# Performance work log

Hardware: AMD Instinct MI355X
Metric: run time of the kernel (lower is better)

The kernel has to match this reference:

```python
import jax, jax.numpy as jnp
import numpy as np

B, N, C = 4, 2048, 768
H = 12
D = C // H  # head_dim = 64
SCALE = D ** -0.5


def setup_inputs() -> dict:
    key = jax.random.key(0)
    ks = jax.random.split(key, 9)
    x_q = jax.random.normal(ks[0], (B, N, C), dtype=jnp.float32)
    x_k = jax.random.normal(ks[1], (B, N, C), dtype=jnp.float32)
    x_v = jax.random.normal(ks[2], (B, N, C), dtype=jnp.float32)
    x_u = jax.random.uniform(ks[3], (B, N, C), dtype=jnp.float32)
    s = C ** -0.5
    Wq = jax.random.normal(ks[4], (C, C), dtype=jnp.float32) * s
    Wk = jax.random.normal(ks[5], (C, C), dtype=jnp.float32) * s
    Wv = jax.random.normal(ks[6], (C, C), dtype=jnp.float32) * s
    Wp = jax.random.normal(ks[7], (C, C), dtype=jnp.float32) * s
    bp = jax.random.normal(ks[8], (C,), dtype=jnp.float32) * 0.01
    return {"x_q": x_q, "x_k": x_k, "x_v": x_v, "x_u": x_u,
            "Wq": Wq, "Wk": Wk, "Wv": Wv, "Wp": Wp, "bp": bp}


def reference(x_q, x_k, x_v, x_u, Wq, Wk, Wv, Wp, bp):
    # Linear projections (torch Linear: y = x @ W.T), split into heads [B,H,N,D]
    def to_heads(x, W):
        y = jnp.einsum('bnc,oc->bno', x, W)
        return y.reshape(B, N, H, D).transpose(0, 2, 1, 3)
    q = to_heads(x_q, Wq) * SCALE
    k = to_heads(x_k, Wk)
    v = to_heads(x_v, Wv)
    # Scores [B,H,N,N]
    attn = jnp.einsum('bhqd,bhkd->bhqk', q, k)
    # Uncertainty map: per-query scalar (mean over channels), broadcast over keys & heads
    uc = jnp.mean(x_u, axis=-1)  # [B,N]
    attn = attn * uc[:, None, :, None]
    attn = jax.nn.softmax(attn, axis=-1)
    out = jnp.einsum('bhqk,bhkd->bhqd', attn, v)
    out = out.transpose(0, 2, 1, 3).reshape(B, N, C)
    return jnp.einsum('bnc,oc->bno', out, Wp) + bp
```

## Files before the change

### kernel.cpp

```cpp
#include <hip/hip_runtime.h>
#include <hip/hip_bf16.h>
#include <cstdint>

#define B_ 4
#define N_ 2048
#define C_ 768
#define H_ 12
#define D_ 64
#define QSCALE 0.18033688011112042f

typedef __bf16 bf16x8 __attribute__((ext_vector_type(8)));
typedef float f32x4 __attribute__((ext_vector_type(4)));
typedef float f32x16 __attribute__((ext_vector_type(16)));

__device__ __forceinline__ unsigned f2bs(float x) {
  unsigned u = __builtin_bit_cast(unsigned, x);
  unsigned r = (u + 0x7fffu + ((u >> 16) & 1u)) >> 16;
  return r;
}

__device__ __forceinline__ bf16x8 ldb8(const unsigned short* p) {
  return __builtin_bit_cast(bf16x8, *(const uint4*)p);
}

__device__ __forceinline__ f32x4 mfma16(bf16x8 a, bf16x8 b, f32x4 c) {
  return __builtin_amdgcn_mfma_f32_16x16x32_bf16(a, b, c, 0, 0, 0);
}

__device__ __forceinline__ f32x16 mfma32(bf16x8 a, bf16x8 b, f32x16 c) {
  return __builtin_amdgcn_mfma_f32_32x32x16_bf16(a, b, c, 0, 0, 0);
}

__device__ __forceinline__ void async16(const unsigned short* g, unsigned short* l) {
  __builtin_amdgcn_global_load_lds(
      (const __attribute__((address_space(1))) unsigned int*)g,
      (__attribute__((address_space(3))) unsigned int*)l, 16, 0, 0);
}

__global__ void prep_kernel(
    const float* __restrict__ xq, const float* __restrict__ xk,
    const float* __restrict__ xv, const float* __restrict__ xu,
    const float* __restrict__ Wq, const float* __restrict__ Wk,
    const float* __restrict__ Wv, const float* __restrict__ Wp,
    unsigned short* __restrict__ dxq, unsigned short* __restrict__ dxk,
    unsigned short* __restrict__ dxv,
    unsigned short* __restrict__ dwq, unsigned short* __restrict__ dwk,
    unsigned short* __restrict__ dwv, unsigned short* __restrict__ dwp,
    float* __restrict__ uc) {
  const int id = blockIdx.x;
  if (id < 18432) {
    const float* s = (id < 6144) ? xq : (id < 12288) ? xk : xv;
    unsigned short* d = (id < 6144) ? dxq : (id < 12288) ? dxk : dxv;
    int i = ((id % 6144) * 256 + threadIdx.x) * 4;
    float4 v = *(const float4*)(s + i);
    ushort4 h;
    h.x = (unsigned short)f2bs(v.x); h.y = (unsigned short)f2bs(v.y);
    h.z = (unsigned short)f2bs(v.z); h.w = (unsigned short)f2bs(v.w);
    *(ushort4*)(d + i) = h;
  } else if (id < 20736) {
    int sub = id - 18432;
    int which = sub / 576;
    const float* s = (which == 0) ? Wq : (which == 1) ? Wk : (which == 2) ? Wv : Wp;
    unsigned short* d = (which == 0) ? dwq : (which == 1) ? dwk : (which == 2) ? dwv : dwp;
    int i = ((sub % 576) * 256 + threadIdx.x) * 4;
    float4 v = *(const float4*)(s + i);
    ushort4 h;
    h.x = (unsigned short)f2bs(v.x); h.y = (unsigned short)f2bs(v.y);
    h.z = (unsigned short)f2bs(v.z); h.w = (unsigned short)f2bs(v.w);
    *(ushort4*)(d + i) = h;
  } else {
    int sub = id - 20736;
    int w = threadIdx.x >> 6, lane = threadIdx.x & 63;
    int row = sub * 4 + w;
    const float* p = xu + (size_t)row * C_;
    float s = 0.f;
#pragma unroll
    for (int i = 0; i < 3; ++i) {
      float4 v = *(const float4*)(p + (i * 64 + lane) * 4);
      s += v.x + v.y + v.z + v.w;
    }
#pragma unroll
    for (int off = 1; off < 64; off <<= 1) s += __shfl_xor(s, off);
    if (lane == 0) uc[row] = s * (1.f / 768.f);
  }
}

__device__ __forceinline__ void gemm_mainloop(
    const unsigned short* __restrict__ A, const unsigned short* __restrict__ W,
    int m0, int n0, unsigned short* Al, unsigned short* Bl,
    int tid, int wm, int wn, int quad, int id15, f32x4 (*acc)[4]) {
  const int wb = tid & 192;
  const unsigned short* ap[4];
  const unsigned short* bp[4];
#pragma unroll
  for (int s = 0; s < 4; ++s) {
    int g = s * 256 + tid;
    int row = (g >> 2) & 127;
    int col = ((g >> 9) << 5) | ((g & 3) << 3);
    ap[s] = A + (size_t)(m0 + row) * C_ + col;
    bp[s] = W + (size_t)(n0 + row) * C_ + col;
  }

  for (int kt = 0; kt < C_; kt += 64) {
    __syncthreads();
#pragma unroll
    for (int s = 0; s < 4; ++s) {
      async16(ap[s] + kt, Al + (s * 256 + wb) * 8);
      async16(bp[s] + kt, Bl + (s * 256 + wb) * 8);
    }
    __syncthreads();

#pragma unroll
    for (int kk = 0; kk < 2; ++kk) {
      bf16x8 af[4], bfr[4];
#pragma unroll
      for (int i = 0; i < 4; ++i)
        af[i]  = ldb8(&Al[kk * 4096 + (wm + i * 16 + id15) * 32 + quad * 8]);
#pragma unroll
      for (int j = 0; j < 4; ++j)
        bfr[j] = ldb8(&Bl[kk * 4096 + (wn + j * 16 + id15) * 32 + quad * 8]);
#pragma unroll
      for (int i = 0; i < 4; ++i)
#pragma unroll
        for (int j = 0; j < 4; ++j)
          acc[i][j] = mfma16(af[i], bfr[j], acc[i][j]);
    }
  }
}

#define TSTR 136
__global__ __launch_bounds__(256, 3) void gemm_qkv(
    const unsigned short* __restrict__ xq, const unsigned short* __restrict__ xk,
    const unsigned short* __restrict__ xv,
    const unsigned short* __restrict__ wq, const unsigned short* __restrict__ wk,
    const unsigned short* __restrict__ wv,
    unsigned short* __restrict__ oq, unsigned short* __restrict__ ok,
    unsigned short* __restrict__ ov, const float* __restrict__ uc) {
  __shared__ __align__(16) unsigned short S[128 * TSTR];
  unsigned short* Al = S;
  unsigned short* Bl = S + 8192;
  const int tid = threadIdx.x;
  const int w = tid >> 6, lane = tid & 63, quad = lane >> 4, id15 = lane & 15;
  const int wm = (w >> 1) << 6, wn = (w & 1) << 6;
  const int id = blockIdx.x;
  const int xcd = id & 7, slot = id >> 3;
  const int n0 = (slot % 6) << 7;
  const int gz = xcd * 24 + slot / 6;
  const int z = gz >> 6, m0 = (gz & 63) << 7;

  const unsigned short* A = (z == 0) ? xq : (z == 1) ? xk : xv;
  const unsigned short* W = (z == 0) ? wq : (z == 1) ? wk : wv;

  f32x4 acc[4][4] = {};
  gemm_mainloop(A, W, m0, n0, Al, Bl, tid, wm, wn, quad, id15, acc);

  if (z == 2) {
    __syncthreads();
#pragma unroll
    for (int i = 0; i < 4; ++i)
#pragma unroll
      for (int j = 0; j < 4; ++j) {
        uint2 u;
        u.x = f2bs(acc[i][j][0]) | (f2bs(acc[i][j][1]) << 16);
        u.y = f2bs(acc[i][j][2]) | (f2bs(acc[i][j][3]) << 16);
        *(uint2*)&S[(wn + j * 16 + id15) * TSTR + wm + i * 16 + quad * 4] = u;
      }
    __syncthreads();
    const int b = m0 >> 11, nb = m0 & (N_ - 1);
#pragma unroll
    for (int s = 0; s < 8; ++s) {
      int c = s * 256 + tid;
      int row = c >> 4, o = (c & 15) << 3;
      *(uint4*)(ov + (size_t)(b * C_ + n0 + row) * N_ + nb + o) = *(const uint4*)&S[row * TSTR + o];
    }
    return;
  }

#pragma unroll
  for (int i = 0; i < 4; ++i) {
#pragma unroll
    for (int j = 0; j < 4; ++j) {
#pragma unroll
      for (int r = 0; r < 4; ++r) {
        int gm = m0 + wm + i * 16 + quad * 4 + r;
        int gn = n0 + wn + j * 16 + id15;
        float v = acc[i][j][r];
        if (z == 0) {
          v *= QSCALE * uc[gm];
          oq[(size_t)gm * C_ + gn] = (unsigned short)f2bs(v);
        } else {
          ok[(size_t)gm * C_ + gn] = (unsigned short)f2bs(v);
        }
      }
    }
  }
}

__global__ __launch_bounds__(256, 4) void gemm_out(
    const unsigned short* __restrict__ ao, const unsigned short* __restrict__ wp,
    float* __restrict__ out, const float* __restrict__ bias) {
  __shared__ __align__(16) unsigned short Al[64 * 64];
  __shared__ __align__(16) unsigned short Bl[128 * 64];
  const int tid = threadIdx.x;
  const int w = tid >> 6, lane = tid & 63, quad = lane >> 4, id15 = lane & 15;
  const int wm = (w >> 1) << 5, wn = (w & 1) << 6;
  const int id = blockIdx.x;
  const int xcd = id & 7, slot = id >> 3;
  const int n0 = (slot % 6) << 7;
  const int m0 = (xcd * 16 + slot / 6) << 6;

  const int wb = tid & 192;
  const unsigned short* ap[2];
#pragma unroll
  for (int s = 0; s < 2; ++s) {
    int g = s * 256 + tid;
    int row = (g >> 2) & 63;
    int col = ((g >> 8) << 5) | ((g & 3) << 3);
    ap[s] = ao + (size_t)(m0 + row) * C_ + col;
  }
  const unsigned short* bp[4];
#pragma unroll
  for (int s = 0; s < 4; ++s) {
    int g = s * 256 + tid;
    int row = (g >> 2) & 127;
    int col = ((g >> 9) << 5) | ((g & 3) << 3);
    bp[s] = wp + (size_t)(n0 + row) * C_ + col;
  }

  f32x4 acc[2][4] = {};
  for (int kt = 0; kt < C_; kt += 64) {
    __syncthreads();
#pragma unroll
    for (int s = 0; s < 2; ++s) async16(ap[s] + kt, Al + (s * 256 + wb) * 8);
#pragma unroll
    for (int s = 0; s < 4; ++s) async16(bp[s] + kt, Bl + (s * 256 + wb) * 8);
    __syncthreads();

#pragma unroll
    for (int kk = 0; kk < 2; ++kk) {
      bf16x8 af[2], bfr[4];
#pragma unroll
      for (int i = 0; i < 2; ++i)
        af[i]  = ldb8(&Al[kk * 2048 + (wm + i * 16 + id15) * 32 + quad * 8]);
#pragma unroll
      for (int j = 0; j < 4; ++j)
        bfr[j] = ldb8(&Bl[kk * 4096 + (wn + j * 16 + id15) * 32 + quad * 8]);
#pragma unroll
      for (int i = 0; i < 2; ++i)
#pragma unroll
        for (int j = 0; j < 4; ++j)
          acc[i][j] = mfma16(af[i], bfr[j], acc[i][j]);
    }
  }

#pragma unroll
  for (int i = 0; i < 2; ++i) {
#pragma unroll
    for (int j = 0; j < 4; ++j) {
#pragma unroll
      for (int r = 0; r < 4; ++r) {
        int gm = m0 + wm + i * 16 + quad * 4 + r;
        int gn = n0 + wn + j * 16 + id15;
        out[(size_t)gm * C_ + gn] = acc[i][j][r] + bias[gn];
      }
    }
  }
}

#define KSTR 72
#define VOFF (64 * KSTR)
#define BUFO (2 * 64 * KSTR)
__global__ __launch_bounds__(256, 3) void attn_kernel(
    const unsigned short* __restrict__ Q, const unsigned short* __restrict__ Kk,
    const unsigned short* __restrict__ Vt, unsigned short* __restrict__ O) {
  __shared__ __align__(16) unsigned short KV[2 * 2 * 64 * KSTR];

  const int tid = threadIdx.x;
  const int w = tid >> 6, lane = tid & 63;
  const int i32 = lane & 31, hi = lane >> 5;
  const int id = blockIdx.x;
  const int xcd = id & 7, slot = id >> 3;
  const int bh = xcd * 6 + (slot >> 4);
  const int qt = slot & 15;
  const int b = bh / H_, h = bh % H_;
  const int q0 = qt * 128 + w * 32;

  bf16x8 qf[4];
#pragma unroll
  for (int s = 0; s < 4; ++s)
    qf[s] = ldb8(Q + (size_t)(b * N_ + q0 + i32) * C_ + h * 64 + s * 16 + hi * 8);

  const uint4 onesu = {0x3F803F80u, 0x3F803F80u, 0x3F803F80u, 0x3F803F80u};
  const bf16x8 onesf = __builtin_bit_cast(bf16x8, onesu);

  f32x16 oacc0 = {}, oacc1 = {}, lacc = {};

  const size_t kbase = (size_t)(b * N_) * C_ + h * 64;
  const size_t vbase = (size_t)(b * C_ + h * 64) * N_;
  const int srow0 = tid >> 3, srow1 = 32 + (tid >> 3);
  const int sseg = (tid & 7) << 3;
  const int addrLow = i32 << 2;
  const int addrHigh = addrLow | 128;

  auto compute = [&](const unsigned short* Kc) {
    const unsigned short* Vc = Kc + VOFF;
#pragma unroll
    for (int t = 0; t < 2; ++t) {
      f32x16 s16 = {};
#pragma unroll
      for (int s = 0; s < 4; ++s) {
        bf16x8 kf = ldb8(Kc + (t * 32 + i32) * KSTR + s * 16 + hi * 8);
        s16 = mfma32(kf, qf[s], s16);
      }
      unsigned Dw[8];
#pragma unroll
      for (int j = 0; j < 8; ++j) {
        float e0 = exp2f(s16[2 * j]);
        float e1 = exp2f(s16[2 * j + 1]);
        unsigned d;
        asm("v_cvt_pk_bf16_f32 %0, %1, %2" : "=v"(d) : "v"(e0), "v"(e1));
        Dw[j] = d;
      }
#pragma unroll
      for (int sl = 0; sl < 2; ++sl) {
        const int bb = sl * 4;
        unsigned L2 = (unsigned)__builtin_amdgcn_ds_bpermute(addrLow, (int)Dw[bb + 2]);
        unsigned L3 = (unsigned)__builtin_amdgcn_ds_bpermute(addrLow, (int)Dw[bb + 3]);
        unsigned H0 = (unsigned)__builtin_amdgcn_ds_bpermute(addrHigh, (int)Dw[bb + 0]);
        unsigned H1 = (unsigned)__builtin_amdgcn_ds_bpermute(addrHigh, (int)Dw[bb + 1]);
        uint4 u;
        u.x = hi ? L2 : Dw[bb + 0];
        u.y = hi ? L3 : Dw[bb + 1];
        u.z = hi ? Dw[bb + 2] : H0;
        u.w = hi ? Dw[bb + 3] : H1;
        bf16x8 pf = __builtin_bit_cast(bf16x8, u);
        lacc = mfma32(pf, onesf, lacc);
        bf16x8 v0 = ldb8(Vc + i32 * KSTR + (2 * t + sl) * 16 + hi * 8);
        bf16x8 v1 = ldb8(Vc + (32 + i32) * KSTR + (2 * t + sl) * 16 + hi * 8);
        oacc0 = mfma32(pf, v0, oacc0);
        oacc1 = mfma32(pf, v1, oacc1);
      }
    }
  };

  {
    uint4 a0 = *(const uint4*)(Kk + kbase + (size_t)srow0 * C_ + sseg);
    uint4 a1 = *(const uint4*)(Kk + kbase + (size_t)srow1 * C_ + sseg);
    uint4 c0 = *(const uint4*)(Vt + vbase + (size_t)srow0 * N_ + sseg);
    uint4 c1 = *(const uint4*)(Vt + vbase + (size_t)srow1 * N_ + sseg);
    *(uint4*)&KV[srow0 * KSTR + sseg] = a0;
    *(uint4*)&KV[srow1 * KSTR + sseg] = a1;
    *(uint4*)&KV[VOFF + srow0 * KSTR + sseg] = c0;
    *(uint4*)&KV[VOFF + srow1 * KSTR + sseg] = c1;
  }

  int cur = 0;
  for (int kc = 0; kc < N_ - 64; kc += 64) {
    const int kcn = kc + 64;
    uint4 a0 = *(const uint4*)(Kk + kbase + (size_t)(kcn + srow0) * C_ + sseg);
    uint4 a1 = *(const uint4*)(Kk + kbase + (size_t)(kcn + srow1) * C_ + sseg);
    uint4 c0 = *(const uint4*)(Vt + vbase + (size_t)srow0 * N_ + kcn + sseg);
    uint4 c1 = *(const uint4*)(Vt + vbase + (size_t)srow1 * N_ + kcn + sseg);

    __syncthreads();

    compute(KV + (cur ? BUFO : 0));

    unsigned short* Kn = KV + (cur ? 0 : BUFO);
    *(uint4*)&Kn[srow0 * KSTR + sseg] = a0;
    *(uint4*)&Kn[srow1 * KSTR + sseg] = a1;
    *(uint4*)&Kn[VOFF + srow0 * KSTR + sseg] = c0;
    *(uint4*)&Kn[VOFF + srow1 * KSTR + sseg] = c1;
    cur ^= 1;
  }
  __syncthreads();
  compute(KV + (cur ? BUFO : 0));

#pragma unroll
  for (int r = 0; r < 16; ++r) {
    float linv = 1.0f / lacc[r];
    int q = q0 + (r & 3) + 8 * (r >> 2) + 4 * hi;
    size_t base = (size_t)(b * N_ + q) * C_ + h * 64 + i32;
    O[base] = (unsigned short)f2bs(oacc0[r] * linv);
    O[base + 32] = (unsigned short)f2bs(oacc1[r] * linv);
  }
}

extern "C" void kernel_launch(void* const* d_in, const int* in_sizes, int n_in,
                              void* d_out, int out_size, void* d_ws, size_t ws_size,
                              hipStream_t stream) {
  const float* x_q = (const float*)d_in[0];
  const float* x_k = (const float*)d_in[1];
  const float* x_v = (const float*)d_in[2];
  const float* x_u = (const float*)d_in[3];
  const float* Wq  = (const float*)d_in[4];
  const float* Wk  = (const float*)d_in[5];
  const float* Wv  = (const float*)d_in[6];
  const float* Wp  = (const float*)d_in[7];
  const float* bp  = (const float*)d_in[8];

  char* ws = (char*)d_ws;
  size_t off = 0;
  auto alloc = [&](size_t bytes) {
    char* p = ws + off;
    off += (bytes + 255) & ~(size_t)255;
    return p;
  };
  unsigned short* wq16 = (unsigned short*)alloc((size_t)C_ * C_ * 2);
  unsigned short* wk16 = (unsigned short*)alloc((size_t)C_ * C_ * 2);
  unsigned short* wv16 = (unsigned short*)alloc((size_t)C_ * C_ * 2);
  unsigned short* wp16 = (unsigned short*)alloc((size_t)C_ * C_ * 2);
  float*          ucp  = (float*)alloc((size_t)B_ * N_ * 4);
  unsigned short* xq16 = (unsigned short*)alloc((size_t)B_ * N_ * C_ * 2);
  unsigned short* xk16 = (unsigned short*)alloc((size_t)B_ * N_ * C_ * 2);
  unsigned short* xv16 = (unsigned short*)alloc((size_t)B_ * N_ * C_ * 2);
  unsigned short* q_s  = (unsigned short*)alloc((size_t)B_ * N_ * C_ * 2);
  unsigned short* k_s  = (unsigned short*)alloc((size_t)B_ * N_ * C_ * 2);
  unsigned short* vT   = (unsigned short*)alloc((size_t)B_ * N_ * C_ * 2);
  unsigned short* ao   = (unsigned short*)alloc((size_t)B_ * N_ * C_ * 2);

  prep_kernel<<<dim3(22784), 256, 0, stream>>>(x_q, x_k, x_v, x_u, Wq, Wk, Wv, Wp,
                                               xq16, xk16, xv16,
                                               wq16, wk16, wv16, wp16, ucp);
  gemm_qkv<<<dim3(1152), 256, 0, stream>>>(xq16, xk16, xv16, wq16, wk16, wv16,
                                           q_s, k_s, vT, ucp);
  attn_kernel<<<dim3(768), 256, 0, stream>>>(q_s, k_s, vT, ao);
  gemm_out<<<dim3(768), 256, 0, stream>>>(ao, wp16, (float*)d_out, bp);
}
```

Baseline: 310.9 us.

## Load V fragments directly from global and use permlane32 swap for P

V is no longer staged through shared memory. Each wave loads its V operand fragments straight from global memory into registers each iteration, which halves LDS usage and the LDS write/read traffic. The ds_bpermute-based lane exchange for the P fragment is replaced by v_permlane32_swap, avoiding LDS-routed permutes. The trade-off is that V loads are now issued redundantly per wave, and their global latency is only partly hidden within the same iteration. The barrier is now a manual lgkmcnt wait followed by s_barrier.

New measurement: 317.2 us. 1.02x slower.

```diff
diff --git a/kernel.cpp b/kernel.cpp
--- a/kernel.cpp
+++ b/kernel.cpp
@@ -268,12 +268,11 @@
 }
 
 #define KSTR 72
-#define VOFF (64 * KSTR)
-#define BUFO (2 * 64 * KSTR)
+#define BUFO (64 * KSTR)
 __global__ __launch_bounds__(256, 3) void attn_kernel(
     const unsigned short* __restrict__ Q, const unsigned short* __restrict__ Kk,
     const unsigned short* __restrict__ Vt, unsigned short* __restrict__ O) {
-  __shared__ __align__(16) unsigned short KV[2 * 2 * 64 * KSTR];
+  __shared__ __align__(16) unsigned short Kl[2 * 64 * KSTR];
 
   const int tid = threadIdx.x;
   const int w = tid >> 6, lane = tid & 63;
@@ -299,11 +298,34 @@
   const size_t vbase = (size_t)(b * C_ + h * 64) * N_;
   const int srow0 = tid >> 3, srow1 = 32 + (tid >> 3);
   const int sseg = (tid & 7) << 3;
-  const int addrLow = i32 << 2;
-  const int addrHigh = addrLow | 128;
-
-  auto compute = [&](const unsigned short* Kc) {
-    const unsigned short* Vc = Kc + VOFF;
+  const unsigned short* vp = Vt + vbase + (size_t)i32 * N_ + hi * 8;
+
+  {
+    uint4 a0 = *(const uint4*)(Kk + kbase + (size_t)srow0 * C_ + sseg);
+    uint4 a1 = *(const uint4*)(Kk + kbase + (size_t)srow1 * C_ + sseg);
+    *(uint4*)&Kl[srow0 * KSTR + sseg] = a0;
+    *(uint4*)&Kl[srow1 * KSTR + sseg] = a1;
+  }
+
+  int cur = 0;
+  for (int kc = 0; kc < N_; kc += 64) {
+    uint4 vr[4][2];
+#pragma unroll
+    for (int ks = 0; ks < 4; ++ks) {
+      vr[ks][0] = *(const uint4*)(vp + kc + ks * 16);
+      vr[ks][1] = *(const uint4*)(vp + 32 * N_ + kc + ks * 16);
+    }
+    const bool last = (kc + 64 >= N_);
+    uint4 a0, a1;
+    if (!last) {
+      a0 = *(const uint4*)(Kk + kbase + (size_t)(kc + 64 + srow0) * C_ + sseg);
+      a1 = *(const uint4*)(Kk + kbase + (size_t)(kc + 64 + srow1) * C_ + sseg);
+    }
+
+    asm volatile("s_waitcnt lgkmcnt(0)" ::: "memory");
+    __builtin_amdgcn_s_barrier();
+
+    const unsigned short* Kc = Kl + (cur ? BUFO : 0);
 #pragma unroll
     for (int t = 0; t < 2; ++t) {
       f32x16 s16 = {};
@@ -324,57 +346,29 @@
 #pragma unroll
       for (int sl = 0; sl < 2; ++sl) {
         const int bb = sl * 4;
-        unsigned L2 = (unsigned)__builtin_amdgcn_ds_bpermute(addrLow, (int)Dw[bb + 2]);
-        unsigned L3 = (unsigned)__builtin_amdgcn_ds_bpermute(addrLow, (int)Dw[bb + 3]);
-        unsigned H0 = (unsigned)__builtin_amdgcn_ds_bpermute(addrHigh, (int)Dw[bb + 0]);
-        unsigned H1 = (unsigned)__builtin_amdgcn_ds_bpermute(addrHigh, (int)Dw[bb + 1]);
+        unsigned x0 = Dw[bb + 0], y0 = Dw[bb + 2];
+        unsigned x1 = Dw[bb + 1], y1 = Dw[bb + 3];
+        asm("v_permlane32_swap_b32 %0, %1" : "+v"(x0), "+v"(y0));
+        asm("v_permlane32_swap_b32 %0, %1" : "+v"(x1), "+v"(y1));
         uint4 u;
-        u.x = hi ? L2 : Dw[bb + 0];
-        u.y = hi ? L3 : Dw[bb + 1];
-        u.z = hi ? Dw[bb + 2] : H0;
-        u.w = hi ? Dw[bb + 3] : H1;
+        u.x = x0;
+        u.y = x1;
+        u.z = y0;
+        u.w = y1;
         bf16x8 pf = __builtin_bit_cast(bf16x8, u);
         lacc = mfma32(pf, onesf, lacc);
-        bf16x8 v0 = ldb8(Vc + i32 * KSTR + (2 * t + sl) * 16 + hi * 8);
-        bf16x8 v1 = ldb8(Vc + (32 + i32) * KSTR + (2 * t + sl) * 16 + hi * 8);
-        oacc0 = mfma32(pf, v0, oacc0);
-        oacc1 = mfma32(pf, v1, oacc1);
-      }
-    }
-  };
-
-  {
-    uint4 a0 = *(const uint4*)(Kk + kbase + (size_t)srow0 * C_ + sseg);
-    uint4 a1 = *(const uint4*)(Kk + kbase + (size_t)srow1 * C_ + sseg);
-    uint4 c0 = *(const uint4*)(Vt + vbase + (size_t)srow0 * N_ + sseg);
-    uint4 c1 = *(const uint4*)(Vt + vbase + (size_t)srow1 * N_ + sseg);
-    *(uint4*)&KV[srow0 * KSTR + sseg] = a0;
-    *(uint4*)&KV[srow1 * KSTR + sseg] = a1;
-    *(uint4*)&KV[VOFF + srow0 * KSTR + sseg] = c0;
-    *(uint4*)&KV[VOFF + srow1 * KSTR + sseg] = c1;
-  }
-
-  int cur = 0;
-  for (int kc = 0; kc < N_ - 64; kc += 64) {
-    const int kcn = kc + 64;
-    uint4 a0 = *(const uint4*)(Kk + kbase + (size_t)(kcn + srow0) * C_ + sseg);
-    uint4 a1 = *(const uint4*)(Kk + kbase + (size_t)(kcn + srow1) * C_ + sseg);
-    uint4 c0 = *(const uint4*)(Vt + vbase + (size_t)srow0 * N_ + kcn + sseg);
-    uint4 c1 = *(const uint4*)(Vt + vbase + (size_t)srow1 * N_ + kcn + sseg);
-
-    __syncthreads();
-
-    compute(KV + (cur ? BUFO : 0));
-
-    unsigned short* Kn = KV + (cur ? 0 : BUFO);
-    *(uint4*)&Kn[srow0 * KSTR + sseg] = a0;
-    *(uint4*)&Kn[srow1 * KSTR + sseg] = a1;
-    *(uint4*)&Kn[VOFF + srow0 * KSTR + sseg] = c0;
-    *(uint4*)&Kn[VOFF + srow1 * KSTR + sseg] = c1;
+        oacc0 = mfma32(pf, __builtin_bit_cast(bf16x8, vr[2 * t + sl][0]), oacc0);
+        oacc1 = mfma32(pf, __builtin_bit_cast(bf16x8, vr[2 * t + sl][1]), oacc1);
+      }
+    }
+
+    if (!last) {
+      unsigned short* Kn = Kl + (cur ? 0 : BUFO);
+      *(uint4*)&Kn[srow0 * KSTR + sseg] = a0;
+      *(uint4*)&Kn[srow1 * KSTR + sseg] = a1;
+    }
     cur ^= 1;
   }
-  __syncthreads();
-  compute(KV + (cur ? BUFO : 0));
 
 #pragma unroll
   for (int r = 0; r < 16; ++r) {
```
